# Performance work log

Measured on AMD Instinct MI355X. Metric: run time of the kernel, lower is better.

The kernel has to match this reference:

```python
import jax, jax.numpy as jnp
import numpy as np
import math

HEADS = 16
HIDDEN = 2048
D_K = HIDDEN // HEADS
BATCH = 2
SEQ = 2048
ROPE_THETA = 10000.0


def make_freqs_cis(seq_len, d_k, theta=ROPE_THETA):
    # Llama rotary frequencies; returned as (seq, d_k//2, 2) = (cos, sin)
    inv_freq = 1.0 / (theta ** (np.arange(0, d_k, 2, dtype=np.float32) / d_k))
    t = np.arange(seq_len, dtype=np.float32)
    ang = np.outer(t, inv_freq)  # (seq, d_k//2)
    return jnp.asarray(np.stack([np.cos(ang), np.sin(ang)], axis=-1))


def setup_inputs() -> dict:
    key = jax.random.key(0)
    ks = jax.random.split(key, 5)
    scale = 1.0 / math.sqrt(HIDDEN)
    return {
        "x": jax.random.normal(ks[0], (BATCH, SEQ, HIDDEN), dtype=jnp.float32),
        "freqs_cis": make_freqs_cis(SEQ, D_K),
        "wq": jax.random.normal(ks[1], (HIDDEN, HIDDEN), dtype=jnp.float32) * scale,
        "wk": jax.random.normal(ks[2], (HIDDEN, HIDDEN), dtype=jnp.float32) * scale,
        "wv": jax.random.normal(ks[3], (HIDDEN, HIDDEN), dtype=jnp.float32) * scale,
        "wo": jax.random.normal(ks[4], (HIDDEN, HIDDEN), dtype=jnp.float32) * scale,
    }


def _apply_rope(t, cos, sin):
    # t: (B, S, h, d_k); cos/sin: (1, S, 1, d_k//2)
    B, S, h, dk = t.shape
    tp = t.reshape(B, S, h, dk // 2, 2)
    t0, t1 = tp[..., 0], tp[..., 1]
    r0 = t0 * cos - t1 * sin
    r1 = t0 * sin + t1 * cos
    return jnp.stack([r0, r1], axis=-1).reshape(B, S, h, dk)


def reference(x, freqs_cis, wq, wk, wv, wo):
    B, S, H = x.shape
    h, dk = HEADS, H // HEADS
    # nn.Linear(bias=False): y = x @ W.T
    q = (x @ wq.T).reshape(B, S, h, dk)
    k = (x @ wk.T).reshape(B, S, h, dk)
    v = (x @ wv.T).reshape(B, S, h, dk)
    cos = freqs_cis[None, :, None, :, 0]
    sin = freqs_cis[None, :, None, :, 1]
    q = _apply_rope(q, cos, sin)
    k = _apply_rope(k, cos, sin)
    # (B, h, S, dk)
    q = q.transpose(0, 2, 1, 3)
    k = k.transpose(0, 2, 1, 3)
    v = v.transpose(0, 2, 1, 3)
    scores = jnp.einsum("bhqd,bhkd->bhqk", q, k) / math.sqrt(dk)
    causal = jnp.tril(jnp.ones((S, S), dtype=bool))
    scores = jnp.where(causal[None, None], scores, -jnp.inf)
    attn = jax.nn.softmax(scores, axis=-1)
    out = jnp.einsum("bhqk,bhkd->bhqd", attn, v)
    out = out.transpose(0, 2, 1, 3).reshape(B, S, H)
    return out @ wo.T
```

## Files before the change

kernel.cpp:

```cpp
#include <hip/hip_runtime.h>

#define SEQ 2048
#define HID 2048
#define NH 16
#define DK 128
#define NTOK 4096

typedef __bf16 bf16x8 __attribute__((ext_vector_type(8)));
typedef float f32x4 __attribute__((ext_vector_type(4)));
typedef float f32x16 __attribute__((ext_vector_type(16)));
typedef unsigned int u32x4 __attribute__((ext_vector_type(4)));

__device__ __forceinline__ unsigned short f2bf(float f) {
  unsigned int u = __builtin_bit_cast(unsigned int, f);
  u += 0x7fffu + ((u >> 16) & 1u);
  return (unsigned short)(u >> 16);
}
__device__ __forceinline__ float bf2f(unsigned int lo16) {
  return __builtin_bit_cast(float, lo16 << 16);
}

__device__ __forceinline__ void async_cp16(const void* g, void* l) {
  __builtin_amdgcn_global_load_lds(
      (__attribute__((address_space(1))) void*)const_cast<void*>(g),
      (__attribute__((address_space(3))) void*)l, 16, 0, 0);
}

__global__ void convert_all_kernel(const float* __restrict__ x,
                                   const float* __restrict__ wq,
                                   const float* __restrict__ wk,
                                   const float* __restrict__ wv,
                                   const float* __restrict__ wo,
                                   const float* __restrict__ fc,
                                   unsigned short* __restrict__ xb,
                                   unsigned short* __restrict__ wqb,
                                   unsigned short* __restrict__ wkb,
                                   unsigned short* __restrict__ wvb,
                                   unsigned short* __restrict__ wob,
                                   unsigned int* __restrict__ fcb) {
  const int bid = blockIdx.x;
  if (bid >= 24576) {
    const int idx = (bid - 24576) * 256 + threadIdx.x;
    const int s = idx >> 6, d = idx & 63;
    const float2 cs = *(const float2*)(fc + s * 128 + 2 * d);
    fcb[idx] = (unsigned int)f2bf(cs.x) | ((unsigned int)f2bf(cs.y) << 16);
    return;
  }
  const float* src;
  unsigned short* dst;
  int base;
  if (bid < 8192) {
    src = x; dst = xb; base = bid;
  } else {
    const int t = (bid - 8192) >> 12;
    base = (bid - 8192) & 4095;
    src = (t == 0) ? wq : (t == 1) ? wk : (t == 2) ? wv : wo;
    dst = (t == 0) ? wqb : (t == 1) ? wkb : (t == 2) ? wvb : wob;
  }
  const int i = base * 256 + threadIdx.x;
  float4 v = ((const float4*)src)[i];
  ushort4 o;
  o.x = f2bf(v.x); o.y = f2bf(v.y); o.z = f2bf(v.z); o.w = f2bf(v.w);
  ((ushort4*)dst)[i] = o;
}

template<bool F32OUT>
__global__ __launch_bounds__(256, 2)
void gemm_bt_kernel(const unsigned short* __restrict__ A,
                    const unsigned short* __restrict__ B,
                    unsigned short* __restrict__ Ob,
                    float* __restrict__ Of,
                    const unsigned int* __restrict__ fcb,
                    const int mode) {
  __shared__ alignas(16) unsigned short As[128 * 64];
  __shared__ alignas(16) unsigned short Bs[128 * 64];

  const int bx = blockIdx.x, by = blockIdx.y;
  const int col0 = bx * 128;
  const int row0 = by * 128;

  const int tid = threadIdx.x;
  const int wave = tid >> 6, lane = tid & 63;
  const int quad = lane >> 4, r = lane & 15;
  const int wm = wave >> 1, wn = wave & 1;
  const int jbase = wave * 256 + lane;

  f32x4 acc[4][4] = {};

  for (int k0 = 0; k0 < HID; k0 += 64) {
    for (int t = 0; t < 4; ++t) {
      const int j = jbase + t * 64;
      const int m = j >> 3;
      const int gc = (j & 7) ^ (m & 7);
      async_cp16(A + (size_t)(row0 + m) * HID + k0 + gc * 8, As + j * 8);
      async_cp16(B + (size_t)(col0 + m) * HID + k0 + gc * 8, Bs + j * 8);
    }
    __syncthreads();
    for (int kk = 0; kk < 2; ++kk) {
      bf16x8 af[4], bfr[4];
      for (int mt = 0; mt < 4; ++mt) {
        const int m = wm * 64 + mt * 16 + r;
        const int slot = (kk * 4 + quad) ^ (m & 7);
        af[mt] = __builtin_bit_cast(bf16x8, *(const u32x4*)(As + m * 64 + slot * 8));
      }
      for (int nt = 0; nt < 4; ++nt) {
        const int n = wn * 64 + nt * 16 + r;
        const int slot = (kk * 4 + quad) ^ (n & 7);
        bfr[nt] = __builtin_bit_cast(bf16x8, *(const u32x4*)(Bs + n * 64 + slot * 8));
      }
      for (int mt = 0; mt < 4; ++mt)
        for (int nt = 0; nt < 4; ++nt)
          acc[mt][nt] = __builtin_amdgcn_mfma_f32_16x16x32_bf16(
              af[mt], bfr[nt], acc[mt][nt], 0, 0, 0);
    }
    __syncthreads();
  }

  if (!F32OUT && mode == 2) {
    for (int mt = 0; mt < 4; ++mt) {
      const int row = row0 + wm * 64 + mt * 16 + quad * 4;
      const int b = row >> 11, s = row & (SEQ - 1);
      for (int nt = 0; nt < 4; ++nt) {
        const int col = col0 + wn * 64 + nt * 16 + r;
        ushort4 pk;
        pk.x = f2bf(acc[mt][nt][0]);
        pk.y = f2bf(acc[mt][nt][1]);
        pk.z = f2bf(acc[mt][nt][2]);
        pk.w = f2bf(acc[mt][nt][3]);
        *(ushort4*)(Ob + ((size_t)(b * HID + col)) * SEQ + s) = pk;
      }
    }
    return;
  }

  if (!F32OUT) {
    const float qs = (mode == 0) ? 0.12751743f : 1.0f;
    for (int mt = 0; mt < 4; ++mt) {
      const int row = row0 + wm * 64 + mt * 16 + quad * 4;
      for (int nt = 0; nt < 4; ++nt) {
        const int col = col0 + wn * 64 + nt * 16 + r;
        const int d = (wn * 64 + nt * 16 + r) >> 1;
        for (int v = 0; v < 4; ++v) {
          const int s = (row + v) & (SEQ - 1);
          const unsigned int u = fcb[s * 64 + d];
          const float c = bf2f(u & 0xffffu), sn = bf2f(u >> 16);
          const float val = acc[mt][nt][v];
          const float par = __shfl_xor(val, 1, 64);
          const float res = (r & 1) ? (par * sn + val * c)
                                    : (val * c - par * sn);
          Ob[(size_t)(row + v) * HID + col] = f2bf(res * qs);
        }
      }
    }
    return;
  }

  for (int mt = 0; mt < 4; ++mt) {
    const int row = row0 + wm * 64 + mt * 16 + quad * 4;
    for (int nt = 0; nt < 4; ++nt) {
      const int col = col0 + wn * 64 + nt * 16 + r;
      for (int v = 0; v < 4; ++v)
        Of[(size_t)(row + v) * HID + col] = acc[mt][nt][v];
    }
  }
}

__global__ __launch_bounds__(256, 2)
void flash_attn_kernel(const unsigned short* __restrict__ Qb,
                       const unsigned short* __restrict__ Kb,
                       const unsigned short* __restrict__ VtG,
                       unsigned short* __restrict__ Ob) {
  __shared__ alignas(16) unsigned short KsA[64 * 128];
  __shared__ alignas(16) unsigned short KsB[64 * 128];
  __shared__ alignas(16) unsigned short VsA[128 * 64];
  __shared__ alignas(16) unsigned short VsB[128 * 64];

  const int bid0 = blockIdx.y * 16 + blockIdx.x;
  const int wid = (bid0 & 7) * 64 + (bid0 >> 3);
  const int bx = wid & 15, bh = wid >> 4;
  const int tid = threadIdx.x, wave = tid >> 6, lane = tid & 63;
  const int l31 = lane & 31, hl = lane >> 5;
  const int qgrp = wave >> 1, ksub = wave & 1;
  const int tokbase = (bh >> 4) * SEQ;
  const int hh = bh & 15;

  auto stage = [&](int kt, unsigned short* Ks, unsigned short* Vs) {
    for (int t = 0; t < 4; ++t) {
      const int j = t * 256 + tid;
      const int n = j >> 4, slot = j & 15;
      const int gc = slot ^ (n & 15);
      async_cp16(Kb + (size_t)(tokbase + kt * 64 + n) * HID + hh * DK + gc * 8,
                 Ks + j * 8);
    }
    for (int t = 0; t < 4; ++t) {
      const int j = t * 256 + tid;
      const int d = j >> 3, slot = j & 7;
      const int gc = slot ^ (d & 7);
      async_cp16(VtG + ((size_t)(bh * DK + d)) * SEQ + kt * 64 + gc * 8,
                 Vs + j * 8);
    }
  };

  for (int phase = 0; phase < 2; ++phase) {
    const int qt = phase ? (31 - bx) : bx;
    const int q0 = qt * 64;
    const int qloc = qgrp * 32 + l31;

    u32x4 qf[8];
    {
      const unsigned short* qrow =
          Qb + (size_t)(tokbase + q0 + qloc) * HID + hh * DK;
#pragma unroll
      for (int ks = 0; ks < 8; ++ks)
        qf[ks] = *(const u32x4*)(qrow + ks * 16 + hl * 8);
    }

    f32x16 o[4] = {};
    float m_i = -__builtin_inff(), l_i = 0.f;

    auto body = [&](const unsigned short* Ks, const unsigned short* Vs,
                    int kt) {
      f32x16 s = {};
      const unsigned short* krow = Ks + (size_t)(ksub * 32 + l31) * 128;
      __builtin_amdgcn_s_setprio(1);
#pragma unroll
      for (int ks = 0; ks < 8; ++ks) {
        const int slot = (ks * 2 + hl) ^ (lane & 15);
        const u32x4 kf = *(const u32x4*)(krow + slot * 8);
        s = __builtin_amdgcn_mfma_f32_32x32x16_bf16(
            __builtin_bit_cast(bf16x8, kf),
            __builtin_bit_cast(bf16x8, qf[ks]), s, 0, 0, 0);
      }
      __builtin_amdgcn_s_setprio(0);

      float sv[16];
#pragma unroll
      for (int r = 0; r < 16; ++r) sv[r] = s[r];
      if (kt == qt) {
#pragma unroll
        for (int r = 0; r < 16; ++r) {
          const int kloc = ksub * 32 + (r & 3) + 8 * (r >> 2) + 4 * hl;
          if (kloc > qloc) sv[r] = -__builtin_inff();
        }
      }

      float mx = fmaxf(fmaxf(fmaxf(sv[0], sv[1]), fmaxf(sv[2], sv[3])),
                       fmaxf(fmaxf(sv[4], sv[5]), fmaxf(sv[6], sv[7])));
      mx = fmaxf(mx,
                 fmaxf(fmaxf(fmaxf(sv[8], sv[9]), fmaxf(sv[10], sv[11])),
                       fmaxf(fmaxf(sv[12], sv[13]), fmaxf(sv[14], sv[15]))));
      mx = fmaxf(mx, __shfl_xor(mx, 32, 64));

      if (!__all(mx <= m_i + 8.f)) {
        const float mnew = fmaxf(m_i, mx);
        const float al = exp2f(m_i - mnew);
        m_i = mnew;
        l_i *= al;
#pragma unroll
        for (int dt = 0; dt < 4; ++dt)
#pragma unroll
          for (int r = 0; r < 16; ++r) o[dt][r] *= al;
      }

      float p[16];
      float rs = 0.f;
#pragma unroll
      for (int r = 0; r < 16; ++r) {
        p[r] = exp2f(fmaxf(sv[r] - m_i, -128.f));
        rs += p[r];
      }
      l_i += rs + __shfl_xor(rs, 32, 64);

      u32x4 af[2];
#pragma unroll
      for (int kk = 0; kk < 2; ++kk) {
        unsigned int a, b2, c2, d2;
        asm("v_cvt_pk_bf16_f32 %0, %1, %2"
            : "=v"(a) : "v"(p[8 * kk + 0]), "v"(p[8 * kk + 1]));
        asm("v_cvt_pk_bf16_f32 %0, %1, %2"
            : "=v"(b2) : "v"(p[8 * kk + 2]), "v"(p[8 * kk + 3]));
        asm("v_cvt_pk_bf16_f32 %0, %1, %2"
            : "=v"(c2) : "v"(p[8 * kk + 4]), "v"(p[8 * kk + 5]));
        asm("v_cvt_pk_bf16_f32 %0, %1, %2"
            : "=v"(d2) : "v"(p[8 * kk + 6]), "v"(p[8 * kk + 7]));
        asm("v_permlane32_swap_b32 %0, %1" : "+v"(a), "+v"(c2));
        asm("v_permlane32_swap_b32 %0, %1" : "+v"(b2), "+v"(d2));
        u32x4 t = {a, b2, c2, d2};
        af[kk] = t;
      }

      __builtin_amdgcn_s_setprio(1);
#pragma unroll
      for (int kk = 0; kk < 2; ++kk)
#pragma unroll
        for (int dt = 0; dt < 4; ++dt) {
          const int d = dt * 32 + l31;
          const int slot = (ksub * 4 + kk * 2 + hl) ^ (d & 7);
          const u32x4 vv = *(const u32x4*)(Vs + (size_t)d * 64 + slot * 8);
          o[dt] = __builtin_amdgcn_mfma_f32_32x32x16_bf16(
              __builtin_bit_cast(bf16x8, af[kk]),
              __builtin_bit_cast(bf16x8, vv), o[dt], 0, 0, 0);
        }
      __builtin_amdgcn_s_setprio(0);
    };

    stage(0, KsA, VsA);
    int kt = 0;
    while (true) {
      __syncthreads();
      if (kt + 1 <= qt) stage(kt + 1, KsB, VsB);
      body(KsA, VsA, kt);
      if (++kt > qt) break;
      __syncthreads();
      if (kt + 1 <= qt) stage(kt + 1, KsA, VsA);
      body(KsB, VsB, kt);
      if (++kt > qt) break;
    }

    __syncthreads();
    float* obuf = (float*)(qgrp == 0 ? (void*)KsA : (void*)VsA);
    float* mlbuf = (float*)KsB;
    if (ksub == 1) {
#pragma unroll
      for (int dt = 0; dt < 4; ++dt)
#pragma unroll
        for (int r = 0; r < 16; ++r) {
          const int qr = (r & 3) + 8 * (r >> 2) + 4 * hl;
          obuf[qr * 128 + dt * 32 + l31] = o[dt][r];
        }
    }
    if (lane < 32) {
      mlbuf[wave * 64 + lane] = m_i;
      mlbuf[wave * 64 + 32 + lane] = l_i;
    }
    __syncthreads();
    if (ksub == 0) {
      float f0[16], f1[16];
#pragma unroll
      for (int r = 0; r < 16; ++r) {
        const int qr = (r & 3) + 8 * (r >> 2) + 4 * hl;
        const float m0 = mlbuf[wave * 64 + qr];
        const float l0 = mlbuf[wave * 64 + 32 + qr];
        const float m1 = mlbuf[(wave + 1) * 64 + qr];
        const float l1 = mlbuf[(wave + 1) * 64 + 32 + qr];
        const float mm = fmaxf(m0, m1);
        const float a0 = exp2f(fmaxf(m0 - mm, -128.f));
        const float a1 = exp2f(fmaxf(m1 - mm, -128.f));
        const float li = 1.f / (l0 * a0 + l1 * a1);
        f0[r] = a0 * li;
        f1[r] = a1 * li;
      }
#pragma unroll
      for (int dt = 0; dt < 4; ++dt)
#pragma unroll
        for (int r = 0; r < 16; ++r) {
          const int qr = (r & 3) + 8 * (r >> 2) + 4 * hl;
          const float om =
              o[dt][r] * f0[r] + obuf[qr * 128 + dt * 32 + l31] * f1[r];
          Ob[(size_t)(tokbase + q0 + qgrp * 32 + qr) * HID + hh * DK +
             dt * 32 + l31] = f2bf(om);
        }
    }
    __syncthreads();
  }
}

extern "C" void kernel_launch(void* const* d_in, const int* in_sizes, int n_in,
                              void* d_out, int out_size, void* d_ws, size_t ws_size,
                              hipStream_t stream) {
  const float* x  = (const float*)d_in[0];
  const float* fc = (const float*)d_in[1];
  const float* wq = (const float*)d_in[2];
  const float* wk = (const float*)d_in[3];
  const float* wv = (const float*)d_in[4];
  const float* wo = (const float*)d_in[5];
  float* out = (float*)d_out;

  unsigned short* xb  = (unsigned short*)d_ws;
  unsigned short* wqb = xb  + (size_t)NTOK * HID;
  unsigned short* wkb = wqb + (size_t)HID * HID;
  unsigned short* wvb = wkb + (size_t)HID * HID;
  unsigned short* wob = wvb + (size_t)HID * HID;
  unsigned short* qb  = wob + (size_t)HID * HID;
  unsigned short* kb  = qb  + (size_t)NTOK * HID;
  unsigned short* vtb = kb  + (size_t)NTOK * HID;
  unsigned short* ab  = vtb + (size_t)NTOK * HID;
  unsigned int*   fcb = (unsigned int*)(ab + (size_t)NTOK * HID);

  convert_all_kernel<<<24576 + 512, 256, 0, stream>>>(
      x, wq, wk, wv, wo, fc, xb, wqb, wkb, wvb, wob, fcb);

  gemm_bt_kernel<false><<<dim3(16, 32), 256, 0, stream>>>(
      xb, wqb, qb, nullptr, fcb, 0);
  gemm_bt_kernel<false><<<dim3(16, 32), 256, 0, stream>>>(
      xb, wkb, kb, nullptr, fcb, 1);
  gemm_bt_kernel<false><<<dim3(16, 32), 256, 0, stream>>>(
      xb, wvb, vtb, nullptr, fcb, 2);

  flash_attn_kernel<<<dim3(16, 32), 256, 0, stream>>>(qb, kb, vtb, ab);

  gemm_bt_kernel<true><<<dim3(16, 32), 256, 0, stream>>>(
      ab, wob, nullptr, out, fcb, 0);
}
```

Before: 376.9 us.

## Restructure flash attention to one query tile per block, single-buffered, higher occupancy

The attention kernel stops pairing two query tiles per block. It now launches one block per (head, query tile), scheduling the longest causal tiles first, and drops the K/V double buffer in favour of a single LDS buffer with a sync before and after each tile. LDS usage is halved and launch bounds go up to 4 blocks per CU, so overlap should come from more resident blocks instead of in-block prefetching. Masking now uses a finite negative value so the clamps in exp2 can be removed. The cost is that no copy overlaps compute inside a block, blocks get uneven work, and the register budget per thread is tighter.

```diff
diff --git a/kernel.cpp b/kernel.cpp
--- a/kernel.cpp
+++ b/kernel.cpp
@@ -165,203 +165,194 @@
   }
 }
 
-__global__ __launch_bounds__(256, 2)
+__global__ __launch_bounds__(256, 4)
 void flash_attn_kernel(const unsigned short* __restrict__ Qb,
                        const unsigned short* __restrict__ Kb,
                        const unsigned short* __restrict__ VtG,
                        unsigned short* __restrict__ Ob) {
-  __shared__ alignas(16) unsigned short KsA[64 * 128];
-  __shared__ alignas(16) unsigned short KsB[64 * 128];
-  __shared__ alignas(16) unsigned short VsA[128 * 64];
-  __shared__ alignas(16) unsigned short VsB[128 * 64];
-
-  const int bid0 = blockIdx.y * 16 + blockIdx.x;
-  const int wid = (bid0 & 7) * 64 + (bid0 >> 3);
-  const int bx = wid & 15, bh = wid >> 4;
+  __shared__ alignas(16) unsigned short Ks[64 * 128];
+  __shared__ alignas(16) unsigned short Vs[128 * 64];
+  __shared__ float Ml[4][64];
+
+  const int bid = blockIdx.x;
+  const int local = bid >> 3;
+  const int qt = 31 - (local >> 2);
+  const int bh = (bid & 7) * 4 + (local & 3);
   const int tid = threadIdx.x, wave = tid >> 6, lane = tid & 63;
   const int l31 = lane & 31, hl = lane >> 5;
   const int qgrp = wave >> 1, ksub = wave & 1;
   const int tokbase = (bh >> 4) * SEQ;
   const int hh = bh & 15;
-
-  auto stage = [&](int kt, unsigned short* Ks, unsigned short* Vs) {
+  const int q0 = qt * 64;
+  const int qloc = qgrp * 32 + l31;
+
+  const float NEG = -30000.f;
+
+  const unsigned short* kp[4];
+  const unsigned short* vp[4];
+#pragma unroll
+  for (int t = 0; t < 4; ++t) {
+    const int j = t * 256 + tid;
+    const int n = j >> 4, slotK = j & 15, gcK = slotK ^ (n & 15);
+    kp[t] = Kb + (size_t)(tokbase + n) * HID + hh * DK + gcK * 8;
+    const int d = j >> 3, slotV = j & 7, gcV = slotV ^ (d & 7);
+    vp[t] = VtG + (size_t)(bh * DK + d) * SEQ + gcV * 8;
+  }
+
+  u32x4 qf[8];
+  {
+    const unsigned short* qrow =
+        Qb + (size_t)(tokbase + q0 + qloc) * HID + hh * DK;
+#pragma unroll
+    for (int ks = 0; ks < 8; ++ks)
+      qf[ks] = *(const u32x4*)(qrow + ks * 16 + hl * 8);
+  }
+
+  f32x16 o[4] = {};
+  float m_i = NEG, l_i = 0.f;
+
+  for (int kt = 0; kt <= qt; ++kt) {
+#pragma unroll
     for (int t = 0; t < 4; ++t) {
-      const int j = t * 256 + tid;
-      const int n = j >> 4, slot = j & 15;
-      const int gc = slot ^ (n & 15);
-      async_cp16(Kb + (size_t)(tokbase + kt * 64 + n) * HID + hh * DK + gc * 8,
-                 Ks + j * 8);
-    }
+      async_cp16(kp[t], Ks + (t * 256 + tid) * 8);
+      kp[t] += 64 * HID;
+    }
+#pragma unroll
     for (int t = 0; t < 4; ++t) {
-      const int j = t * 256 + tid;
-      const int d = j >> 3, slot = j & 7;
-      const int gc = slot ^ (d & 7);
-      async_cp16(VtG + ((size_t)(bh * DK + d)) * SEQ + kt * 64 + gc * 8,
-                 Vs + j * 8);
-    }
-  };
-
-  for (int phase = 0; phase < 2; ++phase) {
-    const int qt = phase ? (31 - bx) : bx;
-    const int q0 = qt * 64;
-    const int qloc = qgrp * 32 + l31;
-
-    u32x4 qf[8];
-    {
-      const unsigned short* qrow =
-          Qb + (size_t)(tokbase + q0 + qloc) * HID + hh * DK;
-#pragma unroll
-      for (int ks = 0; ks < 8; ++ks)
-        qf[ks] = *(const u32x4*)(qrow + ks * 16 + hl * 8);
-    }
-
-    f32x16 o[4] = {};
-    float m_i = -__builtin_inff(), l_i = 0.f;
-
-    auto body = [&](const unsigned short* Ks, const unsigned short* Vs,
-                    int kt) {
-      f32x16 s = {};
-      const unsigned short* krow = Ks + (size_t)(ksub * 32 + l31) * 128;
-      __builtin_amdgcn_s_setprio(1);
-#pragma unroll
-      for (int ks = 0; ks < 8; ++ks) {
-        const int slot = (ks * 2 + hl) ^ (lane & 15);
-        const u32x4 kf = *(const u32x4*)(krow + slot * 8);
-        s = __builtin_amdgcn_mfma_f32_32x32x16_bf16(
-            __builtin_bit_cast(bf16x8, kf),
-            __builtin_bit_cast(bf16x8, qf[ks]), s, 0, 0, 0);
-      }
-      __builtin_amdgcn_s_setprio(0);
-
-      float sv[16];
-#pragma unroll
-      for (int r = 0; r < 16; ++r) sv[r] = s[r];
-      if (kt == qt) {
-#pragma unroll
-        for (int r = 0; r < 16; ++r) {
-          const int kloc = ksub * 32 + (r & 3) + 8 * (r >> 2) + 4 * hl;
-          if (kloc > qloc) sv[r] = -__builtin_inff();
-        }
-      }
-
-      float mx = fmaxf(fmaxf(fmaxf(sv[0], sv[1]), fmaxf(sv[2], sv[3])),
-                       fmaxf(fmaxf(sv[4], sv[5]), fmaxf(sv[6], sv[7])));
-      mx = fmaxf(mx,
-                 fmaxf(fmaxf(fmaxf(sv[8], sv[9]), fmaxf(sv[10], sv[11])),
-                       fmaxf(fmaxf(sv[12], sv[13]), fmaxf(sv[14], sv[15]))));
-      mx = fmaxf(mx, __shfl_xor(mx, 32, 64));
-
-      if (!__all(mx <= m_i + 8.f)) {
-        const float mnew = fmaxf(m_i, mx);
-        const float al = exp2f(m_i - mnew);
-        m_i = mnew;
-        l_i *= al;
-#pragma unroll
-        for (int dt = 0; dt < 4; ++dt)
-#pragma unroll
-          for (int r = 0; r < 16; ++r) o[dt][r] *= al;
-      }
-
-      float p[16];
-      float rs = 0.f;
+      async_cp16(vp[t], Vs + (t * 256 + tid) * 8);
+      vp[t] += 64;
+    }
+    __syncthreads();
+
+    f32x16 s = {};
+    const unsigned short* krow = Ks + (size_t)(ksub * 32 + l31) * 128;
+    __builtin_amdgcn_s_setprio(1);
+#pragma unroll
+    for (int ks = 0; ks < 8; ++ks) {
+      const int slot = (ks * 2 + hl) ^ (lane & 15);
+      const u32x4 kf = *(const u32x4*)(krow + slot * 8);
+      s = __builtin_amdgcn_mfma_f32_32x32x16_bf16(
+          __builtin_bit_cast(bf16x8, kf),
+          __builtin_bit_cast(bf16x8, qf[ks]), s, 0, 0, 0);
+    }
+    __builtin_amdgcn_s_setprio(0);
+
+    float sv[16];
+#pragma unroll
+    for (int r = 0; r < 16; ++r) sv[r] = s[r];
+    if (kt == qt) {
 #pragma unroll
       for (int r = 0; r < 16; ++r) {
-        p[r] = exp2f(fmaxf(sv[r] - m_i, -128.f));
-        rs += p[r];
-      }
-      l_i += rs + __shfl_xor(rs, 32, 64);
-
-      u32x4 af[2];
-#pragma unroll
-      for (int kk = 0; kk < 2; ++kk) {
-        unsigned int a, b2, c2, d2;
-        asm("v_cvt_pk_bf16_f32 %0, %1, %2"
-            : "=v"(a) : "v"(p[8 * kk + 0]), "v"(p[8 * kk + 1]));
-        asm("v_cvt_pk_bf16_f32 %0, %1, %2"
-            : "=v"(b2) : "v"(p[8 * kk + 2]), "v"(p[8 * kk + 3]));
-        asm("v_cvt_pk_bf16_f32 %0, %1, %2"
-            : "=v"(c2) : "v"(p[8 * kk + 4]), "v"(p[8 * kk + 5]));
-        asm("v_cvt_pk_bf16_f32 %0, %1, %2"
-            : "=v"(d2) : "v"(p[8 * kk + 6]), "v"(p[8 * kk + 7]));
-        asm("v_permlane32_swap_b32 %0, %1" : "+v"(a), "+v"(c2));
-        asm("v_permlane32_swap_b32 %0, %1" : "+v"(b2), "+v"(d2));
-        u32x4 t = {a, b2, c2, d2};
-        af[kk] = t;
-      }
-
-      __builtin_amdgcn_s_setprio(1);
-#pragma unroll
-      for (int kk = 0; kk < 2; ++kk)
-#pragma unroll
-        for (int dt = 0; dt < 4; ++dt) {
-          const int d = dt * 32 + l31;
-          const int slot = (ksub * 4 + kk * 2 + hl) ^ (d & 7);
-          const u32x4 vv = *(const u32x4*)(Vs + (size_t)d * 64 + slot * 8);
-          o[dt] = __builtin_amdgcn_mfma_f32_32x32x16_bf16(
-              __builtin_bit_cast(bf16x8, af[kk]),
-              __builtin_bit_cast(bf16x8, vv), o[dt], 0, 0, 0);
-        }
-      __builtin_amdgcn_s_setprio(0);
-    };
-
-    stage(0, KsA, VsA);
-    int kt = 0;
-    while (true) {
-      __syncthreads();
-      if (kt + 1 <= qt) stage(kt + 1, KsB, VsB);
-      body(KsA, VsA, kt);
-      if (++kt > qt) break;
-      __syncthreads();
-      if (kt + 1 <= qt) stage(kt + 1, KsA, VsA);
-      body(KsB, VsB, kt);
-      if (++kt > qt) break;
-    }
+        const int kloc = ksub * 32 + (r & 3) + 8 * (r >> 2) + 4 * hl;
+        if (kloc > qloc) sv[r] = NEG;
+      }
+    }
+
+    float t0 = fmaxf(fmaxf(sv[0], sv[1]), sv[2]);
+    float t1 = fmaxf(fmaxf(sv[3], sv[4]), sv[5]);
+    float t2 = fmaxf(fmaxf(sv[6], sv[7]), sv[8]);
+    float t3 = fmaxf(fmaxf(sv[9], sv[10]), sv[11]);
+    float t4 = fmaxf(fmaxf(sv[12], sv[13]), sv[14]);
+    float mx = fmaxf(fmaxf(fmaxf(t0, t1), t2),
+                     fmaxf(fmaxf(t3, t4), sv[15]));
+    mx = fmaxf(mx, __shfl_xor(mx, 32, 64));
+
+    if (!__all(mx <= m_i + 8.f)) {
+      const float mnew = fmaxf(m_i, mx);
+      const float al = exp2f(m_i - mnew);
+      m_i = mnew;
+      l_i *= al;
+#pragma unroll
+      for (int dt = 0; dt < 4; ++dt)
+#pragma unroll
+        for (int r = 0; r < 16; ++r) o[dt][r] *= al;
+    }
+
+    float p[16];
+    float rs = 0.f;
+#pragma unroll
+    for (int r = 0; r < 16; ++r) {
+      p[r] = exp2f(sv[r] - m_i);
+      rs += p[r];
+    }
+    l_i += rs + __shfl_xor(rs, 32, 64);
+
+    u32x4 af[2];
+#pragma unroll
+    for (int kk = 0; kk < 2; ++kk) {
+      unsigned int a, b2, c2, d2;
+      asm("v_cvt_pk_bf16_f32 %0, %1, %2"
+          : "=v"(a) : "v"(p[8 * kk + 0]), "v"(p[8 * kk + 1]));
+      asm("v_cvt_pk_bf16_f32 %0, %1, %2"
+          : "=v"(b2) : "v"(p[8 * kk + 2]), "v"(p[8 * kk + 3]));
+      asm("v_cvt_pk_bf16_f32 %0, %1, %2"
+          : "=v"(c2) : "v"(p[8 * kk + 4]), "v"(p[8 * kk + 5]));
+      asm("v_cvt_pk_bf16_f32 %0, %1, %2"
+          : "=v"(d2) : "v"(p[8 * kk + 6]), "v"(p[8 * kk + 7]));
+      asm("v_permlane32_swap_b32 %0, %1" : "+v"(a), "+v"(c2));
+      asm("v_permlane32_swap_b32 %0, %1" : "+v"(b2), "+v"(d2));
+      u32x4 t = {a, b2, c2, d2};
+      af[kk] = t;
+    }
+
+    __builtin_amdgcn_s_setprio(1);
+#pragma unroll
+    for (int kk = 0; kk < 2; ++kk)
+#pragma unroll
+      for (int dt = 0; dt < 4; ++dt) {
+        const int d = dt * 32 + l31;
+        const int slot = (ksub * 4 + kk * 2 + hl) ^ (d & 7);
+        const u32x4 vv = *(const u32x4*)(Vs + (size_t)d * 64 + slot * 8);
+        o[dt] = __builtin_amdgcn_mfma_f32_32x32x16_bf16(
+            __builtin_bit_cast(bf16x8, af[kk]),
+            __builtin_bit_cast(bf16x8, vv), o[dt], 0, 0, 0);
+      }
+    __builtin_amdgcn_s_setprio(0);
 
     __syncthreads();
-    float* obuf = (float*)(qgrp == 0 ? (void*)KsA : (void*)VsA);
-    float* mlbuf = (float*)KsB;
-    if (ksub == 1) {
-#pragma unroll
-      for (int dt = 0; dt < 4; ++dt)
-#pragma unroll
-        for (int r = 0; r < 16; ++r) {
-          const int qr = (r & 3) + 8 * (r >> 2) + 4 * hl;
-          obuf[qr * 128 + dt * 32 + l31] = o[dt][r];
-        }
-    }
-    if (lane < 32) {
-      mlbuf[wave * 64 + lane] = m_i;
-      mlbuf[wave * 64 + 32 + lane] = l_i;
-    }
-    __syncthreads();
-    if (ksub == 0) {
-      float f0[16], f1[16];
+  }
+
+  float* obuf = (float*)(qgrp == 0 ? (void*)Ks : (void*)Vs);
+  if (ksub == 1) {
+#pragma unroll
+    for (int dt = 0; dt < 4; ++dt)
 #pragma unroll
       for (int r = 0; r < 16; ++r) {
         const int qr = (r & 3) + 8 * (r >> 2) + 4 * hl;
-        const float m0 = mlbuf[wave * 64 + qr];
-        const float l0 = mlbuf[wave * 64 + 32 + qr];
-        const float m1 = mlbuf[(wave + 1) * 64 + qr];
-        const float l1 = mlbuf[(wave + 1) * 64 + 32 + qr];
-        const float mm = fmaxf(m0, m1);
-        const float a0 = exp2f(fmaxf(m0 - mm, -128.f));
-        const float a1 = exp2f(fmaxf(m1 - mm, -128.f));
-        const float li = 1.f / (l0 * a0 + l1 * a1);
-        f0[r] = a0 * li;
-        f1[r] = a1 * li;
-      }
-#pragma unroll
-      for (int dt = 0; dt < 4; ++dt)
-#pragma unroll
-        for (int r = 0; r < 16; ++r) {
-          const int qr = (r & 3) + 8 * (r >> 2) + 4 * hl;
-          const float om =
-              o[dt][r] * f0[r] + obuf[qr * 128 + dt * 32 + l31] * f1[r];
-          Ob[(size_t)(tokbase + q0 + qgrp * 32 + qr) * HID + hh * DK +
-             dt * 32 + l31] = f2bf(om);
-        }
-    }
-    __syncthreads();
+        obuf[qr * 128 + dt * 32 + l31] = o[dt][r];
+      }
+  }
+  if (lane < 32) {
+    Ml[wave][lane] = m_i;
+    Ml[wave][32 + lane] = l_i;
+  }
+  __syncthreads();
+  if (ksub == 0) {
+    float f0[16], f1[16];
+#pragma unroll
+    for (int r = 0; r < 16; ++r) {
+      const int qr = (r & 3) + 8 * (r >> 2) + 4 * hl;
+      const float m0 = Ml[wave][qr];
+      const float l0 = Ml[wave][32 + qr];
+      const float m1 = Ml[wave + 1][qr];
+      const float l1 = Ml[wave + 1][32 + qr];
+      const float mm = fmaxf(m0, m1);
+      const float a0 = exp2f(m0 - mm);
+      const float a1 = exp2f(m1 - mm);
+      const float li = 1.f / (l0 * a0 + l1 * a1);
+      f0[r] = a0 * li;
+      f1[r] = a1 * li;
+    }
+#pragma unroll
+    for (int dt = 0; dt < 4; ++dt)
+#pragma unroll
+      for (int r = 0; r < 16; ++r) {
+        const int qr = (r & 3) + 8 * (r >> 2) + 4 * hl;
+        const float om =
+            o[dt][r] * f0[r] + obuf[qr * 128 + dt * 32 + l31] * f1[r];
+        Ob[(size_t)(tokbase + q0 + qgrp * 32 + qr) * HID + hh * DK +
+           dt * 32 + l31] = f2bf(om);
+      }
   }
 }
 
@@ -397,7 +388,7 @@
   gemm_bt_kernel<false><<<dim3(16, 32), 256, 0, stream>>>(
       xb, wvb, vtb, nullptr, fcb, 2);
 
-  flash_attn_kernel<<<dim3(16, 32), 256, 0, stream>>>(qb, kb, vtb, ab);
+  flash_attn_kernel<<<dim3(1024), 256, 0, stream>>>(qb, kb, vtb, ab);
 
   gemm_bt_kernel<true><<<dim3(16, 32), 256, 0, stream>>>(
       ab, wob, nullptr, out, fcb, 0);
```

New measurement: 430.4 us. 14.2% more time.
